# Kernel optimization log

Measured on AMD Instinct MI355X. Metric: run time of the kernel, lower is better.

## Reference

```python
import jax, jax.numpy as jnp
import numpy as np

B = 4096
D = 1024
NUM_CLASSES = 100
TEMPERATURE = 0.5
EPS = 1e-12  # matches F.normalize default eps


def setup_inputs() -> dict:
    key = jax.random.key(0)
    k1, k2, k3 = jax.random.split(key, 3)
    emb_i = jax.random.normal(k1, (B, D), dtype=jnp.float32)
    emb_j = jax.random.normal(k2, (B, D), dtype=jnp.float32)
    labels = jax.random.randint(k3, (B,), 0, NUM_CLASSES, dtype=jnp.int32)
    return {"emb_i": emb_i, "emb_j": emb_j, "labels": labels}


def _l2_normalize(x):
    # F.normalize(x, dim=1): x / max(||x||, eps)
    n = jnp.sqrt(jnp.sum(x * x, axis=1, keepdims=True))
    return x / jnp.maximum(n, EPS)


def reference(emb_i, emb_j, labels):
    z_i = _l2_normalize(emb_i)
    z_j = _l2_normalize(emb_j)
    reps = jnp.concatenate([z_i, z_j], axis=0)          # [2B, D]
    # cosine similarity of already-unit vectors == dot product (GEMM instead
    # of the O(N^2 D) broadcasted elementwise form in the torch code)
    sim = jnp.einsum("nd,md->nm", reps, reps)           # [2B, 2B]

    n2 = 2 * B
    neg_mask = 1.0 - jnp.eye(n2, dtype=sim.dtype)       # exclude self-pairs
    label_t = jnp.concatenate([labels, labels], axis=0)  # [2B]
    ws = (label_t[:, None] == label_t[None, :]).astype(sim.dtype) * neg_mask

    e = jnp.exp(sim / TEMPERATURE)                      # [2B, 2B]
    nominator = jnp.sum(ws * e, axis=1)                 # [2B]
    denominator = jnp.sum(neg_mask * e, axis=1)         # [2B]
    loss_partial = -jnp.log(nominator / denominator)
    return jnp.sum(loss_partial) / (2 * B)
```

## Files before the change

### kernel.cpp

```cpp
#include <hip/hip_runtime.h>
#include <hip/hip_bf16.h>
#include <hip/hip_fp8.h>


#define BHALF 4096
#define N2 8192
#define DK 1024
#define TILE 128
#define BKB 64
#define NTILE 64
#define NBLK 2080

typedef __attribute__((ext_vector_type(16))) float f32x16;
typedef __attribute__((ext_vector_type(4))) int v4i;
typedef __attribute__((ext_vector_type(8))) int v8i;
typedef unsigned char u8;

#define EXP_SCALE 2.8853900817779268f
#define UNIT_SCALE 0x7f7f7f7f

#define WAITVM(n) asm volatile("s_waitcnt vmcnt(" #n ")" ::: "memory")
#define BAR()     asm volatile("s_barrier" ::: "memory")

__global__ __launch_bounds__(256) void normalize_kernel(
    const float* __restrict__ emb_i, const float* __restrict__ emb_j,
    u8* __restrict__ reps, float* __restrict__ nomden,
    float* __restrict__ out) {
    int r = blockIdx.x;
    int t = threadIdx.x;
    int idx = r * 256 + t;
    if (idx < 2 * N2) nomden[idx] = 0.0f;
    if (idx == 0) out[0] = 0.0f;
    const float* src = (r < BHALF) ? (emb_i + (size_t)r * DK)
                                   : (emb_j + (size_t)(r - BHALF) * DK);
    float4 v = ((const float4*)src)[t];
    float s = v.x * v.x + v.y * v.y + v.z * v.z + v.w * v.w;
#pragma unroll
    for (int m = 1; m <= 32; m <<= 1) s += __shfl_xor(s, m, 64);
    __shared__ float red[4];
    if ((t & 63) == 0) red[t >> 6] = s;
    __syncthreads();
    float tot = red[0] + red[1] + red[2] + red[3];
    float scale = 1.0f / fmaxf(sqrtf(tot), 1e-12f);
    __hip_fp8_e4m3 q0(v.x * scale), q1(v.y * scale),
                   q2(v.z * scale), q3(v.w * scale);
    uchar4 o = make_uchar4(q0.__x, q1.__x, q2.__x, q3.__x);
    ((uchar4*)(reps + (size_t)r * DK))[t] = o;
}

__global__ __launch_bounds__(256, 4) void gemm_loss_kernel(
    const u8* __restrict__ reps, const int* __restrict__ labels,
    float* __restrict__ nom, float* __restrict__ den) {
    __shared__ __align__(16) u8 A_s[2][TILE * BKB];
    __shared__ __align__(16) u8 B_s[2][TILE * BKB];

    int rem = blockIdx.x;
    int bi = 0;
    while (rem >= NTILE - bi) { rem -= NTILE - bi; ++bi; }
    int bj = bi + rem;
    int rowBase = bi * TILE;
    int colBase = bj * TILE;

    int tid = threadIdx.x;
    int w = tid >> 6;
    int lane = tid & 63;
    int wm = w >> 1, wn = w & 1;
    int hk = lane >> 5;
    int l31 = lane & 31;

    f32x16 acc[2][2];
#pragma unroll
    for (int i = 0; i < 2; ++i)
#pragma unroll
        for (int j = 0; j < 2; ++j)
#pragma unroll
            for (int r = 0; r < 16; ++r) acc[i][j][r] = 0.0f;

    int srow = lane >> 2;
    int sbg = (lane & 3) ^ ((srow ^ (srow >> 2)) & 3);
    const u8* gA = reps + (size_t)(rowBase + w * 32 + srow) * DK + sbg * 16;
    const u8* gB = reps + (size_t)(colBase + w * 32 + srow) * DK + sbg * 16;

    int rswz = (l31 ^ (l31 >> 2)) & 3;
    unsigned aLo[2], aHi[2], bLo[2], bHi[2];
#pragma unroll
    for (int i = 0; i < 2; ++i) {
        int ra = (wm * 64 + i * 32 + l31) * BKB;
        aLo[i] = ra + (((2 * hk) ^ rswz) << 4);
        aHi[i] = ra + (((2 * hk + 1) ^ rswz) << 4);
        int rb = (wn * 64 + i * 32 + l31) * BKB;
        bLo[i] = rb + (((2 * hk) ^ rswz) << 4);
        bHi[i] = rb + (((2 * hk + 1) ^ rswz) << 4);
    }

#define STAGE(buf, kt)                                                       \
    {                                                                        \
        _Pragma("unroll")                                                    \
        for (int c = 0; c < 2; ++c) {                                        \
            int chunk = 2 * w + c;                                           \
            __builtin_amdgcn_global_load_lds(                                \
                (const __attribute__((address_space(1))) void*)              \
                    (gA + (size_t)c * 16 * DK + (kt) * BKB),                 \
                (__attribute__((address_space(3))) void*)                    \
                    &A_s[buf][chunk * 1024], 16, 0, 0);                      \
            __builtin_amdgcn_global_load_lds(                                \
                (const __attribute__((address_space(1))) void*)              \
                    (gB + (size_t)c * 16 * DK + (kt) * BKB),                 \
                (__attribute__((address_space(3))) void*)                    \
                    &B_s[buf][chunk * 1024], 16, 0, 0);                      \
        }                                                                    \
    }
#define COMPUTE(buf)                                                         \
    {                                                                        \
        v8i aF[2], bF[2];                                                    \
        _Pragma("unroll")                                                    \
        for (int i = 0; i < 2; ++i) {                                        \
            v4i alo = *(const v4i*)&A_s[buf][aLo[i]];                        \
            v4i ahi = *(const v4i*)&A_s[buf][aHi[i]];                        \
            aF[i] = __builtin_shufflevector(alo, ahi, 0,1,2,3,4,5,6,7);      \
            v4i blo = *(const v4i*)&B_s[buf][bLo[i]];                        \
            v4i bhi = *(const v4i*)&B_s[buf][bHi[i]];                        \
            bF[i] = __builtin_shufflevector(blo, bhi, 0,1,2,3,4,5,6,7);      \
        }                                                                    \
        _Pragma("unroll")                                                    \
        for (int i = 0; i < 2; ++i)                                          \
            _Pragma("unroll")                                                \
            for (int j = 0; j < 2; ++j)                                      \
                acc[i][j] = __builtin_amdgcn_mfma_scale_f32_32x32x64_f8f6f4( \
                    aF[i], bF[j], acc[i][j], 0, 0,                           \
                    0, UNIT_SCALE, 0, UNIT_SCALE);                           \
    }

    STAGE(0, 0)
    STAGE(1, 1)
    for (int kt = 0; kt < 12; kt += 2) {
        WAITVM(16); BAR();
        COMPUTE(0)
        BAR();
        STAGE(0, kt + 2)
        WAITVM(16); BAR();
        COMPUTE(1)
        BAR();
        STAGE(1, kt + 3)
    }
    WAITVM(16); BAR();
    COMPUTE(0)
    BAR();
    STAGE(0, 14)
    WAITVM(16); BAR();
    COMPUTE(1)
    BAR();
    STAGE(1, 15)
    WAITVM(16); BAR();
    COMPUTE(0)
    WAITVM(0); BAR();
    COMPUTE(1)
#undef STAGE
#undef COMPUTE

    bool offd = (bi != bj);
    int lc[2], gcol[2];
#pragma unroll
    for (int j = 0; j < 2; ++j) {
        gcol[j] = colBase + wn * 64 + j * 32 + l31;
        lc[j] = labels[gcol[j] & (BHALF - 1)];
    }
    float vD[32], vN[32];
    float colD[2] = {0.f, 0.f}, colN[2] = {0.f, 0.f};
#pragma unroll
    for (int i = 0; i < 2; ++i) {
#pragma unroll
        for (int reg = 0; reg < 16; ++reg) {
            int rowIn = (reg & 3) + 8 * (reg >> 2) + 4 * hk;
            int grow = rowBase + wm * 64 + i * 32 + rowIn;
            int labr = labels[grow & (BHALF - 1)];
            float rD = 0.f, rN = 0.f;
#pragma unroll
            for (int j = 0; j < 2; ++j) {
                float e = exp2f(acc[i][j][reg] * EXP_SCALE);
                if (grow == gcol[j]) e = 0.f;
                bool m = (lc[j] == labr);
                rD += e; if (m) rN += e;
                colD[j] += e; if (m) colN[j] += e;
            }
            vD[i * 16 + reg] = rD;
            vN[i * 16 + reg] = rN;
        }
    }
#pragma unroll
    for (int step = 0; step < 5; ++step) {
        const int m = 16 >> step;
        const int h = 16 >> step;
        bool up = (l31 & m) != 0;
#pragma unroll
        for (int k = 0; k < h; ++k) {
            float sD = up ? vD[k] : vD[k + h];
            float sN = up ? vN[k] : vN[k + h];
            float kD = up ? vD[k + h] : vD[k];
            float kN = up ? vN[k + h] : vN[k];
            vD[k] = kD + __shfl_xor(sD, m, 64);
            vN[k] = kN + __shfl_xor(sN, m, 64);
        }
    }
    {
        int grow = rowBase + wm * 64 + (l31 >> 4) * 32 +
                   ((l31 & 3) + 8 * ((l31 >> 2) & 3) + 4 * hk);
        atomicAdd(&den[grow], vD[0]);
        atomicAdd(&nom[grow], vN[0]);
    }
    if (offd) {
#pragma unroll
        for (int j = 0; j < 2; ++j) {
            float cd = colD[j] + __shfl_xor(colD[j], 32, 64);
            float cn = colN[j] + __shfl_xor(colN[j], 32, 64);
            if (hk == 0) {
                atomicAdd(&den[gcol[j]], cd);
                atomicAdd(&nom[gcol[j]], cn);
            }
        }
    }
}

__global__ __launch_bounds__(256) void finalize_kernel(
    const float* __restrict__ nom, const float* __restrict__ den,
    float* __restrict__ out) {
    int idx = blockIdx.x * 256 + threadIdx.x;
    int t = threadIdx.x;
    float s = 0.f;
    if (idx < N2) s = logf(den[idx]) - logf(nom[idx]);
#pragma unroll
    for (int m = 1; m <= 32; m <<= 1) s += __shfl_xor(s, m, 64);
    __shared__ float red[4];
    if ((t & 63) == 0) red[t >> 6] = s;
    __syncthreads();
    if (t == 0)
        atomicAdd(out, (red[0] + red[1] + red[2] + red[3]) / (float)N2);
}

extern "C" void kernel_launch(void* const* d_in, const int* in_sizes, int n_in,
                              void* d_out, int out_size, void* d_ws, size_t ws_size,
                              hipStream_t stream) {
    const float* emb_i = (const float*)d_in[0];
    const float* emb_j = (const float*)d_in[1];
    const int* labels  = (const int*)d_in[2];
    float* out = (float*)d_out;

    char* ws = (char*)d_ws;
    u8* reps   = (u8*)ws;
    float* nom = (float*)(ws + (size_t)N2 * DK);
    float* den = nom + N2;

    normalize_kernel<<<N2, 256, 0, stream>>>(emb_i, emb_j, reps, nom, out);
    gemm_loss_kernel<<<NBLK, 256, 0, stream>>>(reps, labels, nom, den);
    finalize_kernel<<<(N2 + 255) / 256, 256, 0, stream>>>(nom, den, out);
}
```

Measured before the change: 138.7 us.

## Fuse finalize into GEMM via last-block counter and use wave-per-row normalize

Removes the separate finalize kernel launch: each GEMM block increments a global counter after a fence, and the last block reads the accumulated nom/den and writes the loss directly. The normalize kernel now processes one row per wavefront (4 rows per block), so the row reduction needs only wave shuffles and no shared-memory barrier. This saves a launch and a block-level sync, but leaves the final log reduction to a single block running serially at the tail.

```diff
diff --git a/kernel.cpp b/kernel.cpp
--- a/kernel.cpp
+++ b/kernel.cpp
@@ -24,33 +24,39 @@
 
 __global__ __launch_bounds__(256) void normalize_kernel(
     const float* __restrict__ emb_i, const float* __restrict__ emb_j,
-    u8* __restrict__ reps, float* __restrict__ nomden,
-    float* __restrict__ out) {
-    int r = blockIdx.x;
-    int t = threadIdx.x;
-    int idx = r * 256 + t;
+    u8* __restrict__ reps, float* __restrict__ nomden) {
+    int idx = blockIdx.x * 256 + threadIdx.x;
     if (idx < 2 * N2) nomden[idx] = 0.0f;
-    if (idx == 0) out[0] = 0.0f;
+    if (idx == 2 * N2) ((unsigned*)nomden)[2 * N2] = 0u;
+    int r = blockIdx.x * 4 + (threadIdx.x >> 6);
+    int lane = threadIdx.x & 63;
     const float* src = (r < BHALF) ? (emb_i + (size_t)r * DK)
                                    : (emb_j + (size_t)(r - BHALF) * DK);
-    float4 v = ((const float4*)src)[t];
-    float s = v.x * v.x + v.y * v.y + v.z * v.z + v.w * v.w;
+    const float4* srcv = (const float4*)src;
+    float4 v[4];
+    float s = 0.f;
+#pragma unroll
+    for (int k = 0; k < 4; ++k) {
+        v[k] = srcv[k * 64 + lane];
+        s += v[k].x * v[k].x + v[k].y * v[k].y +
+             v[k].z * v[k].z + v[k].w * v[k].w;
+    }
 #pragma unroll
     for (int m = 1; m <= 32; m <<= 1) s += __shfl_xor(s, m, 64);
-    __shared__ float red[4];
-    if ((t & 63) == 0) red[t >> 6] = s;
-    __syncthreads();
-    float tot = red[0] + red[1] + red[2] + red[3];
-    float scale = 1.0f / fmaxf(sqrtf(tot), 1e-12f);
-    __hip_fp8_e4m3 q0(v.x * scale), q1(v.y * scale),
-                   q2(v.z * scale), q3(v.w * scale);
-    uchar4 o = make_uchar4(q0.__x, q1.__x, q2.__x, q3.__x);
-    ((uchar4*)(reps + (size_t)r * DK))[t] = o;
+    float scale = 1.0f / fmaxf(sqrtf(s), 1e-12f);
+    uchar4* dst = (uchar4*)(reps + (size_t)r * DK);
+#pragma unroll
+    for (int k = 0; k < 4; ++k) {
+        __hip_fp8_e4m3 q0(v[k].x * scale), q1(v[k].y * scale),
+                       q2(v[k].z * scale), q3(v[k].w * scale);
+        dst[k * 64 + lane] = make_uchar4(q0.__x, q1.__x, q2.__x, q3.__x);
+    }
 }
 
 __global__ __launch_bounds__(256, 4) void gemm_loss_kernel(
     const u8* __restrict__ reps, const int* __restrict__ labels,
-    float* __restrict__ nom, float* __restrict__ den) {
+    float* __restrict__ nom, float* __restrict__ den,
+    unsigned* __restrict__ counter, float* __restrict__ out) {
     __shared__ __align__(16) u8 A_s[2][TILE * BKB];
     __shared__ __align__(16) u8 B_s[2][TILE * BKB];
 
@@ -219,22 +225,32 @@
             }
         }
     }
-}
-
-__global__ __launch_bounds__(256) void finalize_kernel(
-    const float* __restrict__ nom, const float* __restrict__ den,
-    float* __restrict__ out) {
-    int idx = blockIdx.x * 256 + threadIdx.x;
-    int t = threadIdx.x;
-    float s = 0.f;
-    if (idx < N2) s = logf(den[idx]) - logf(nom[idx]);
-#pragma unroll
-    for (int m = 1; m <= 32; m <<= 1) s += __shfl_xor(s, m, 64);
-    __shared__ float red[4];
-    if ((t & 63) == 0) red[t >> 6] = s;
+
+    __threadfence();
+    __shared__ unsigned lastS;
+    if (tid == 0) {
+        unsigned prev = __hip_atomic_fetch_add(
+            counter, 1u, __ATOMIC_ACQ_REL, __HIP_MEMORY_SCOPE_AGENT);
+        lastS = (prev == NBLK - 1) ? 1u : 0u;
+    }
     __syncthreads();
-    if (t == 0)
-        atomicAdd(out, (red[0] + red[1] + red[2] + red[3]) / (float)N2);
+    if (lastS) {
+        float s = 0.f;
+        for (int r = tid; r < N2; r += 256) {
+            float dn = __hip_atomic_load(&den[r], __ATOMIC_RELAXED,
+                                         __HIP_MEMORY_SCOPE_AGENT);
+            float nm = __hip_atomic_load(&nom[r], __ATOMIC_RELAXED,
+                                         __HIP_MEMORY_SCOPE_AGENT);
+            s += logf(dn) - logf(nm);
+        }
+#pragma unroll
+        for (int m = 1; m <= 32; m <<= 1) s += __shfl_xor(s, m, 64);
+        __shared__ float red[4];
+        if ((tid & 63) == 0) red[tid >> 6] = s;
+        __syncthreads();
+        if (tid == 0)
+            out[0] = (red[0] + red[1] + red[2] + red[3]) / (float)N2;
+    }
 }
 
 extern "C" void kernel_launch(void* const* d_in, const int* in_sizes, int n_in,
@@ -249,8 +265,9 @@
     u8* reps   = (u8*)ws;
     float* nom = (float*)(ws + (size_t)N2 * DK);
     float* den = nom + N2;
-
-    normalize_kernel<<<N2, 256, 0, stream>>>(emb_i, emb_j, reps, nom, out);
-    gemm_loss_kernel<<<NBLK, 256, 0, stream>>>(reps, labels, nom, den);
-    finalize_kernel<<<(N2 + 255) / 256, 256, 0, stream>>>(nom, den, out);
+    unsigned* cnt = (unsigned*)(den + N2);
+
+    normalize_kernel<<<2048, 256, 0, stream>>>(emb_i, emb_j, reps, nom);
+    gemm_loss_kernel<<<NBLK, 256, 0, stream>>>(reps, labels, nom, den,
+                                               cnt, out);
 }
```

Measured after the change: 417.6 us. 3.01x slower.

## Normalize one row per wavefront and remap GEMM tiles to XCD-contiguous chunks

Applied to the files above, without the earlier changes.

The normalize kernel now handles four rows per 256-thread block, one row per 64-lane wavefront. This removes the shared-memory reduction and block barrier, and each lane loads four float4s instead of one. Separately, the GEMM block index is permuted so that consecutive tiles go to the same XCD (g&7 picks a 260-tile chunk), which is meant to improve L2 reuse of A/B panels on MI355X's multi-die layout. Zeroing of nom/den still covers 2048*256 = 2*N2 entries, so the init stays correct.

```diff
diff --git a/kernel.cpp b/kernel.cpp
--- a/kernel.cpp
+++ b/kernel.cpp
@@ -26,26 +26,32 @@
     const float* __restrict__ emb_i, const float* __restrict__ emb_j,
     u8* __restrict__ reps, float* __restrict__ nomden,
     float* __restrict__ out) {
-    int r = blockIdx.x;
-    int t = threadIdx.x;
-    int idx = r * 256 + t;
+    int idx = blockIdx.x * 256 + threadIdx.x;
     if (idx < 2 * N2) nomden[idx] = 0.0f;
     if (idx == 0) out[0] = 0.0f;
+    int r = blockIdx.x * 4 + (threadIdx.x >> 6);
+    int lane = threadIdx.x & 63;
     const float* src = (r < BHALF) ? (emb_i + (size_t)r * DK)
                                    : (emb_j + (size_t)(r - BHALF) * DK);
-    float4 v = ((const float4*)src)[t];
-    float s = v.x * v.x + v.y * v.y + v.z * v.z + v.w * v.w;
+    const float4* srcv = (const float4*)src;
+    float4 v[4];
+    float s = 0.f;
+#pragma unroll
+    for (int k = 0; k < 4; ++k) {
+        v[k] = srcv[k * 64 + lane];
+        s += v[k].x * v[k].x + v[k].y * v[k].y +
+             v[k].z * v[k].z + v[k].w * v[k].w;
+    }
 #pragma unroll
     for (int m = 1; m <= 32; m <<= 1) s += __shfl_xor(s, m, 64);
-    __shared__ float red[4];
-    if ((t & 63) == 0) red[t >> 6] = s;
-    __syncthreads();
-    float tot = red[0] + red[1] + red[2] + red[3];
-    float scale = 1.0f / fmaxf(sqrtf(tot), 1e-12f);
-    __hip_fp8_e4m3 q0(v.x * scale), q1(v.y * scale),
-                   q2(v.z * scale), q3(v.w * scale);
-    uchar4 o = make_uchar4(q0.__x, q1.__x, q2.__x, q3.__x);
-    ((uchar4*)(reps + (size_t)r * DK))[t] = o;
+    float scale = 1.0f / fmaxf(sqrtf(s), 1e-12f);
+    uchar4* dst = (uchar4*)(reps + (size_t)r * DK);
+#pragma unroll
+    for (int k = 0; k < 4; ++k) {
+        __hip_fp8_e4m3 q0(v[k].x * scale), q1(v[k].y * scale),
+                       q2(v[k].z * scale), q3(v[k].w * scale);
+        dst[k * 64 + lane] = make_uchar4(q0.__x, q1.__x, q2.__x, q3.__x);
+    }
 }
 
 __global__ __launch_bounds__(256, 4) void gemm_loss_kernel(
@@ -54,7 +60,8 @@
     __shared__ __align__(16) u8 A_s[2][TILE * BKB];
     __shared__ __align__(16) u8 B_s[2][TILE * BKB];
 
-    int rem = blockIdx.x;
+    int g = blockIdx.x;
+    int rem = (g & 7) * 260 + (g >> 3);
     int bi = 0;
     while (rem >= NTILE - bi) { rem -= NTILE - bi; ++bi; }
     int bj = bi + rem;
@@ -250,7 +257,7 @@
     float* nom = (float*)(ws + (size_t)N2 * DK);
     float* den = nom + N2;
 
-    normalize_kernel<<<N2, 256, 0, stream>>>(emb_i, emb_j, reps, nom, out);
+    normalize_kernel<<<2048, 256, 0, stream>>>(emb_i, emb_j, reps, nom, out);
     gemm_loss_kernel<<<NBLK, 256, 0, stream>>>(reps, labels, nom, den);
     finalize_kernel<<<(N2 + 255) / 256, 256, 0, stream>>>(nom, den, out);
 }
```

Result: faster. 132.9 us (-4.2%).
